# Performance work log

Measured on AMD Instinct MI355X. Metric: run time of the kernel, lower is better.

The kernel has to match this reference:

```python
import jax, jax.numpy as jnp
import numpy as np

V, E, H, O = 50000, 300, 512, 5
B, T = 256, 200
PAD = 1


def _uniform(key, shape, stdv):
    return jax.random.uniform(key, shape, jnp.float32, -stdv, stdv)


def setup_inputs() -> dict:
    key = jax.random.key(0)
    ks = jax.random.split(key, 12)
    stdv = 1.0 / np.sqrt(H)
    embed = _uniform(ks[0], (V, E), 1.0)
    embed = embed.at[PAD].set(0.0)  # padding_idx=1 row is zero
    Wi = _uniform(ks[1], (H, E + H), stdv); bi = _uniform(ks[2], (H,), stdv)
    Wf = _uniform(ks[3], (H, E + H), stdv); bf = _uniform(ks[4], (H,), stdv)
    Wg = _uniform(ks[5], (H, E + H), stdv); bg = _uniform(ks[6], (H,), stdv)
    Wo = _uniform(ks[7], (H, E + H), stdv); bo = _uniform(ks[8], (H,), stdv)
    stdv_o = 1.0 / np.sqrt(H)
    W_out = _uniform(ks[9], (O, H), stdv_o); b_out = _uniform(ks[10], (O,), stdv_o)
    x = jax.random.randint(ks[11], (B, T), 0, V, dtype=jnp.int32).astype(jnp.int64)
    return {"x": x, "embed": embed, "Wi": Wi, "bi": bi, "Wf": Wf, "bf": bf,
            "Wg": Wg, "bg": bg, "Wo": Wo, "bo": bo, "W_out": W_out, "b_out": b_out}


def _forward(x, embed, Wi, bi, Wf, bf, Wg, bg, Wo, bo, W_out, b_out):
    Bm, Tm = x.shape
    Hm = Wi.shape[0]
    emb = embed[x]  # [B, T, E]

    def step(carry, e_t):
        h, c = carry
        xs = jnp.concatenate([h, e_t], axis=1)  # [B, H+E] (prev_h first, as in torch cat)
        i = jax.nn.sigmoid(xs @ Wi.T + bi)
        f = jax.nn.sigmoid(xs @ Wf.T + bf)
        o = jax.nn.sigmoid(xs @ Wo.T + bo)
        g = jnp.tanh(xs @ Wg.T + bg)
        c = f * c + i * g
        h = jnp.tanh(c) * o
        return (h, c), h

    h0 = jnp.zeros((Bm, Hm), emb.dtype)
    c0 = jnp.zeros((Bm, Hm), emb.dtype)
    (_, _), hs = jax.lax.scan(step, (h0, c0), emb.transpose(1, 0, 2))  # hs: [T, B, H]
    outputs = hs.transpose(1, 0, 2)  # [B, T, H]
    pad = (x == PAD)[:, :, None]
    outputs = jnp.where(pad, 0.0, outputs)
    lengths = jnp.sum(x != PAD, axis=1)
    idx = lengths - 1 + jnp.arange(Bm) * Tm
    final = outputs.reshape(-1, Hm)[idx]  # [B, H]
    # Dropout(p=0.5) in eval mode -> identity
    logits = final @ W_out.T + b_out
    return logits


def reference(x, embed, Wi, bi, Wf, bf, Wg, bg, Wo, bo, W_out, b_out):
    return _forward(x, embed, Wi, bi, Wf, bf, Wg, bg, Wo, bo, W_out, b_out)
```

## Files before the change

kernel.cpp:

```cpp
#include <hip/hip_runtime.h>
#include <hip/hip_bf16.h>
#include <stdint.h>

#define E_SZ 300
#define H_SZ 512
#define O_SZ 5
#define B_SZ 256
#define T_SZ 200
#define PAD_IDX 1

#define KH 512
#define KE 320
#define KTOT 832
#define XS_W 812
#define NK 26
#define NKH 16
#define NKE 10

#define NRG 8
#define ROWS 32
#define NSPLIT 32
#define NW 16
#define WGS 256
#define THREADS 512

#define HROW_PAD 520
#define HROW_B 1040
#define HBUF_HALF (B_SZ * H_SZ)

typedef __bf16  bf16x8 __attribute__((ext_vector_type(8)));
typedef float   f32x4  __attribute__((ext_vector_type(4)));
typedef uint32_t u32x4 __attribute__((ext_vector_type(4)));

__device__ __forceinline__ float fsig(float x) { return 1.0f / (1.0f + __expf(-x)); }
__device__ __forceinline__ float ftanh_(float x) {
    float ax = fabsf(x);
    float e  = __expf(-2.0f * ax);
    float r  = (1.0f - e) / (1.0f + e);
    return x < 0.0f ? -r : r;
}


__global__ void k_pack(const float* __restrict__ Wi, const float* __restrict__ Wf,
                       const float* __restrict__ Wg, const float* __restrict__ Wo,
                       __hip_bfloat16* __restrict__ Wp) {
    int idx = blockIdx.x * blockDim.x + threadIdx.x;
    int total = 4 * H_SZ * KTOT;
    for (int i = idx; i < total; i += gridDim.x * blockDim.x) {
        int k  = i % KTOT;
        int gn = i / KTOT;
        int g = gn >> 9, n = gn & 511;
        const float* W = (g == 0) ? Wi : (g == 1) ? Wf : (g == 2) ? Wg : Wo;
        float v = 0.0f;
        if (k < KH) v = W[n * XS_W + k];
        else { int e = k - KH; if (e < E_SZ) v = W[n * XS_W + KH + e]; }
        Wp[(size_t)gn * KTOT + k] = __float2bfloat16(v);
    }
}

__global__ void k_gather(const int* __restrict__ x, const float* __restrict__ embed,
                         __hip_bfloat16* __restrict__ ebf) {
    int cid = blockIdx.x * blockDim.x + threadIdx.x;
    const int nch = T_SZ * B_SZ * (KE / 8);
    if (cid >= nch) return;
    int ch = cid % (KE / 8);
    int tb = cid / (KE / 8);
    int b = tb % B_SZ;
    int t = tb / B_SZ;
    int row = x[b * T_SZ + t];
    const float* er = embed + (size_t)row * E_SZ;
    __hip_bfloat16 v[8];
    int e0 = ch * 8;
#pragma unroll
    for (int j = 0; j < 8; ++j) {
        int e = e0 + j;
        float f = (e < E_SZ) ? er[e] : 0.0f;
        v[j] = __float2bfloat16(f);
    }
    *reinterpret_cast<ulonglong2*>(ebf + ((size_t)t * B_SZ + b) * KE + e0) =
        *reinterpret_cast<const ulonglong2*>(v);
}

__global__ void k_misc(const int* __restrict__ x, float* __restrict__ final_h,
                       int* __restrict__ tcap, int* __restrict__ flags,
                       int* __restrict__ cns) {
    int tid = blockIdx.x * blockDim.x + threadIdx.x;
    int n = gridDim.x * blockDim.x;
    for (int i = tid; i < B_SZ * H_SZ; i += n) final_h[i] = 0.0f;
    if (tid < NRG * NSPLIT) flags[tid] = 0;
    if (tid < 16) cns[tid] = 0;
    if (tid < B_SZ) {
        int len = 0;
        for (int t = 0; t < T_SZ; ++t) len += (x[tid * T_SZ + t] != PAD_IDX);
        int tf = (len > 0) ? (len - 1) : 0;
        tcap[tid] = (x[tid * T_SZ + tf] == PAD_IDX) ? -1 : tf;
    }
}

__global__ void __launch_bounds__(THREADS, 2)
k_lstm(const __hip_bfloat16* __restrict__ Wp, const __hip_bfloat16* __restrict__ ebf,
       const float* __restrict__ bi, const float* __restrict__ bfv,
       const float* __restrict__ bg, const float* __restrict__ bo,
       __hip_bfloat16* __restrict__ hbuf, float* __restrict__ final_h,
       const int* __restrict__ tcap, int* __restrict__ flags,
       int* __restrict__ cns) {
    __shared__ __align__(16) __hip_bfloat16 h_lds[ROWS * HROW_PAD];
    __shared__ float pre_lds[4][ROWS][NW + 1];
    __shared__ int s_meta[3];

    const int tid  = threadIdx.x;
    const int wave = tid >> 6;
    const int lane = tid & 63;
    const int l15  = lane & 15;
    const int l4   = lane >> 4;
    const int g    = wave & 3;
    const int rh   = wave >> 2;

    if (tid == 0) {
        uint32_t xcc;
        asm volatile("s_getreg_b32 %0, hwreg(HW_REG_XCC_ID)" : "=s"(xcc));
        xcc &= 7;
        int ticket = __hip_atomic_fetch_add(&cns[xcc], 1, __ATOMIC_RELAXED,
                                            __HIP_MEMORY_SCOPE_AGENT);
        __hip_atomic_fetch_add(&cns[8], 1, __ATOMIC_RELEASE,
                               __HIP_MEMORY_SCOPE_AGENT);
        while (__hip_atomic_load(&cns[8], __ATOMIC_RELAXED,
                                 __HIP_MEMORY_SCOPE_AGENT) < WGS)
            __builtin_amdgcn_s_sleep(8);
        (void)__hip_atomic_load(&cns[8], __ATOMIC_ACQUIRE,
                                __HIP_MEMORY_SCOPE_AGENT);
        int bal = 1;
        for (int i = 0; i < 8; ++i)
            bal &= (__hip_atomic_load(&cns[i], __ATOMIC_RELAXED,
                                      __HIP_MEMORY_SCOPE_AGENT) == NSPLIT);
        s_meta[0] = bal ? (int)xcc : (int)(blockIdx.x & 7);
        s_meta[1] = bal ? ticket : (int)(blockIdx.x >> 3);
        s_meta[2] = bal;
    }
    __syncthreads();
    const int rg   = s_meta[0];
    const int ns   = s_meta[1];
    const int fast = s_meta[2];
    const int b0   = rg * ROWS;
    const int n0   = ns * NW;

    bf16x8 wreg[NK];
    {
        const __hip_bfloat16* wB =
            Wp + ((size_t)(g * H_SZ + n0 + l15)) * KTOT + l4 * 8;
#pragma unroll
        for (int kk = 0; kk < NK; ++kk)
            wreg[kk] = *reinterpret_cast<const bf16x8*>(wB + kk * 32);
    }

    const int er  = tid >> 3;
    const int ec  = (tid & 7) * 2;
    const int enn = n0 + ec;
    const int ebb = b0 + er;
    float c0r = 0.f, c1r = 0.f;
    float bi0 = 0, bf0 = 0, bg0 = 0, bo0 = 0, bi1 = 0, bf1 = 0, bg1 = 0, bo1 = 0;
    int tc = -2;
    if (tid < 256) {
        bi0 = bi[enn];     bf0 = bfv[enn];     bg0 = bg[enn];     bo0 = bo[enn];
        bi1 = bi[enn + 1]; bf1 = bfv[enn + 1]; bg1 = bg[enn + 1]; bo1 = bo[enn + 1];
        tc = tcap[ebb];
    }

    int* const fpoll = flags + rg * NSPLIT + (lane & 31);
    int* const fmine = flags + rg * NSPLIT + ns;
    char* const lw   = (char*)(&h_lds[0]) + (wave * 4) * HROW_B;
    const char* hl_a = (const char*)(&h_lds[0]) + (rh * 16 + l15) * HROW_B + l4 * 16;

#pragma unroll 1
    for (int t = 0; t < T_SZ; ++t) {
        f32x4 acc0 = {0.f, 0.f, 0.f, 0.f};
        f32x4 acc1 = {0.f, 0.f, 0.f, 0.f};
        const __hip_bfloat16* ea =
            ebf + ((size_t)t * B_SZ + b0 + rh * 16 + l15) * KE + l4 * 8;
#pragma unroll
        for (int kk = 0; kk < NKE; ++kk) {
            bf16x8 a = *reinterpret_cast<const bf16x8*>(ea + kk * 32);
            if (kk & 1) acc1 = __builtin_amdgcn_mfma_f32_16x16x32_bf16(a, wreg[NKH + kk], acc1, 0, 0, 0);
            else        acc0 = __builtin_amdgcn_mfma_f32_16x16x32_bf16(a, wreg[NKH + kk], acc0, 0, 0, 0);
        }
        if (t > 0) {
            const uint32_t want = (uint32_t)t;
            uint32_t fv;
            if (fast) {
                for (;;) {
                    asm volatile("global_load_dword %0, %1, off sc0\n\t"
                                 "s_waitcnt vmcnt(0)"
                                 : "=&v"(fv)
                                 : "v"((uint64_t)(uintptr_t)fpoll) : "memory");
                    if (__all(fv >= want)) break;
                    __builtin_amdgcn_s_sleep(1);
                }
            } else {
                for (;;) {
                    fv = (uint32_t)__hip_atomic_load(fpoll, __ATOMIC_RELAXED,
                                                     __HIP_MEMORY_SCOPE_AGENT);
                    if (__all(fv >= want)) break;
                    __builtin_amdgcn_s_sleep(2);
                }
            }
            const char* hb = (const char*)hbuf +
                             (size_t)((t - 1) & 1) * (HBUF_HALF * 2);
            if (fast) {
                u32x4 q0, q1, q2, q3;
                const char* dp = hb + (size_t)(b0 + wave * 4) * 1024 + lane * 16;
                asm volatile(
                    "global_load_dwordx4 %0, %4, off sc0\n\t"
                    "global_load_dwordx4 %1, %4, off offset:1024 sc0\n\t"
                    "global_load_dwordx4 %2, %4, off offset:2048 sc0\n\t"
                    "global_load_dwordx4 %3, %4, off offset:3072 sc0\n\t"
                    "s_waitcnt vmcnt(0)"
                    : "=&v"(q0), "=&v"(q1), "=&v"(q2), "=&v"(q3)
                    : "v"((uint64_t)(uintptr_t)dp) : "memory");
                *reinterpret_cast<u32x4*>(lw + lane * 16)              = q0;
                *reinterpret_cast<u32x4*>(lw + HROW_B + lane * 16)     = q1;
                *reinterpret_cast<u32x4*>(lw + 2 * HROW_B + lane * 16) = q2;
                *reinterpret_cast<u32x4*>(lw + 3 * HROW_B + lane * 16) = q3;
            } else {
                uint32_t dep = fv;
                asm volatile("" : "+v"(dep));
                const uint64_t* qp =
                    (const uint64_t*)(hb + (size_t)(b0 + wave * 4) * 1024) +
                    lane + (dep >> 16);
#pragma unroll
                for (int k = 0; k < 4; ++k) {
                    uint64_t a = __hip_atomic_load(qp + k * 128, __ATOMIC_RELAXED,
                                                   __HIP_MEMORY_SCOPE_AGENT);
                    uint64_t b = __hip_atomic_load(qp + k * 128 + 64, __ATOMIC_RELAXED,
                                                   __HIP_MEMORY_SCOPE_AGENT);
                    *reinterpret_cast<uint64_t*>(lw + k * HROW_B + lane * 8)       = a;
                    *reinterpret_cast<uint64_t*>(lw + k * HROW_B + 512 + lane * 8) = b;
                }
            }
            __syncthreads();
#pragma unroll
            for (int kk = 0; kk < NKH; ++kk) {
                bf16x8 a = *reinterpret_cast<const bf16x8*>(hl_a + kk * 64);
                if (kk & 1) acc1 = __builtin_amdgcn_mfma_f32_16x16x32_bf16(a, wreg[kk], acc1, 0, 0, 0);
                else        acc0 = __builtin_amdgcn_mfma_f32_16x16x32_bf16(a, wreg[kk], acc0, 0, 0, 0);
            }
        }
        f32x4 acc = acc0 + acc1;
#pragma unroll
        for (int j = 0; j < 4; ++j)
            pre_lds[g][rh * 16 + l4 * 4 + j][l15] = acc[j];
        __syncthreads();
        if (tid < 256) {
            float pi0 = pre_lds[0][er][ec]     + bi0;
            float pf_ = pre_lds[1][er][ec]     + bf0;
            float pg0 = pre_lds[2][er][ec]     + bg0;
            float po0 = pre_lds[3][er][ec]     + bo0;
            float pi1 = pre_lds[0][er][ec + 1] + bi1;
            float pf1 = pre_lds[1][er][ec + 1] + bf1;
            float pg1 = pre_lds[2][er][ec + 1] + bg1;
            float po1 = pre_lds[3][er][ec + 1] + bo1;
            float i0 = fsig(pi0), f0 = fsig(pf_), g0v = ftanh_(pg0), o0 = fsig(po0);
            float i1 = fsig(pi1), f1 = fsig(pf1), g1v = ftanh_(pg1), o1 = fsig(po1);
            c0r = f0 * c0r + i0 * g0v;
            c1r = f1 * c1r + i1 * g1v;
            float h0 = ftanh_(c0r) * o0;
            float h1 = ftanh_(c1r) * o1;
            uint32_t pk =
                (uint32_t)__builtin_bit_cast(uint16_t, __float2bfloat16(h0)) |
                ((uint32_t)__builtin_bit_cast(uint16_t, __float2bfloat16(h1)) << 16);
            uint32_t* hw = (uint32_t*)((char*)hbuf +
                           (size_t)(t & 1) * (HBUF_HALF * 2) +
                           ((size_t)ebb * H_SZ + enn) * 2);
            if (fast)
                __hip_atomic_store(hw, pk, __ATOMIC_RELAXED,
                                   __HIP_MEMORY_SCOPE_WORKGROUP);
            else
                __hip_atomic_store(hw, pk, __ATOMIC_RELAXED,
                                   __HIP_MEMORY_SCOPE_AGENT);
            if (t == tc) {
                final_h[(size_t)ebb * H_SZ + enn]     = h0;
                final_h[(size_t)ebb * H_SZ + enn + 1] = h1;
            }
        }
        __syncthreads();
        if (tid == 0) {
            if (fast)
                __hip_atomic_store(fmine, t + 1, __ATOMIC_RELAXED,
                                   __HIP_MEMORY_SCOPE_WORKGROUP);
            else
                __hip_atomic_store(fmine, t + 1, __ATOMIC_RELAXED,
                                   __HIP_MEMORY_SCOPE_AGENT);
        }
    }
}

__global__ void k_out(const float* __restrict__ fin, const float* __restrict__ Wout,
                      const float* __restrict__ bout, float* __restrict__ out) {
    int b = blockIdx.x;
    int lane = threadIdx.x;
    float s0 = 0, s1 = 0, s2 = 0, s3 = 0, s4 = 0;
    const float* fr = fin + (size_t)b * H_SZ;
    for (int n = lane; n < H_SZ; n += 64) {
        float h = fr[n];
        s0 += h * Wout[0 * H_SZ + n];
        s1 += h * Wout[1 * H_SZ + n];
        s2 += h * Wout[2 * H_SZ + n];
        s3 += h * Wout[3 * H_SZ + n];
        s4 += h * Wout[4 * H_SZ + n];
    }
#pragma unroll
    for (int off = 32; off >= 1; off >>= 1) {
        s0 += __shfl_down(s0, off);
        s1 += __shfl_down(s1, off);
        s2 += __shfl_down(s2, off);
        s3 += __shfl_down(s3, off);
        s4 += __shfl_down(s4, off);
    }
    if (lane == 0) {
        out[b * O_SZ + 0] = s0 + bout[0];
        out[b * O_SZ + 1] = s1 + bout[1];
        out[b * O_SZ + 2] = s2 + bout[2];
        out[b * O_SZ + 3] = s3 + bout[3];
        out[b * O_SZ + 4] = s4 + bout[4];
    }
}

extern "C" void kernel_launch(void* const* d_in, const int* in_sizes, int n_in,
                              void* d_out, int out_size, void* d_ws, size_t ws_size,
                              hipStream_t stream) {
    const int*   x     = (const int*)d_in[0];
    const float* embed = (const float*)d_in[1];
    const float* Wi    = (const float*)d_in[2];
    const float* bi    = (const float*)d_in[3];
    const float* Wf    = (const float*)d_in[4];
    const float* bfv   = (const float*)d_in[5];
    const float* Wg    = (const float*)d_in[6];
    const float* bg    = (const float*)d_in[7];
    const float* Wo    = (const float*)d_in[8];
    const float* bo    = (const float*)d_in[9];
    const float* Wout  = (const float*)d_in[10];
    const float* bout  = (const float*)d_in[11];
    float* out = (float*)d_out;

    char* ws = (char*)d_ws;
    size_t off = 0;
    auto alloc = [&](size_t bytes) {
        void* p = ws + off;
        off = (off + bytes + 255) & ~(size_t)255;
        return p;
    };
    __hip_bfloat16* Wp   = (__hip_bfloat16*)alloc((size_t)4 * H_SZ * KTOT * 2);
    __hip_bfloat16* ebf  = (__hip_bfloat16*)alloc((size_t)T_SZ * B_SZ * KE * 2);
    __hip_bfloat16* hbuf = (__hip_bfloat16*)alloc((size_t)2 * HBUF_HALF * 2);
    float* finh          = (float*)alloc((size_t)B_SZ * H_SZ * 4);
    int*   tcap          = (int*)alloc((size_t)B_SZ * 4);
    int*   flags         = (int*)alloc((size_t)NRG * NSPLIT * 4);
    int*   cns           = (int*)alloc((size_t)16 * 4);
    (void)ws_size; (void)in_sizes; (void)n_in; (void)out_size;

    k_pack<<<832, 256, 0, stream>>>(Wi, Wf, Wg, Wo, Wp);
    k_gather<<<(T_SZ * B_SZ * (KE / 8) + 255) / 256, 256, 0, stream>>>(x, embed, ebf);
    k_misc<<<128, 256, 0, stream>>>(x, finh, tcap, flags, cns);

    void* args[] = { &Wp, &ebf, &bi, &bfv, &bg, &bo, &hbuf, &finh, &tcap,
                     &flags, &cns };
    hipLaunchCooperativeKernel((void*)k_lstm, dim3(WGS), dim3(THREADS), args, 0, stream);

    k_out<<<B_SZ, 64, 0, stream>>>(finh, Wout, bout, out);
}
```

Measured before the change: 877.9 us.

## Interleave gate weights per column and compute LSTM cell in-register via shuffles

Repacks the weight matrix so the four gates of each hidden column are adjacent, and switches the partition to 16 row-groups of 16 batch rows with 32 columns each. MFMA outputs are transposed across lanes with xor-shuffles so each lane holds i/f/g/o for one element, removing the pre-activation LDS staging and one barrier per step. Flag polling moves to a single wave followed by a barrier, and hidden-state stores become 16-bit volatile writes. This halves the h rows each workgroup loads per step but doubles the number of groups that must synchronise. The slow-path LDS writes include a redundant, oddly computed store.

Result: slower. 1.004 ms (+14.4%).

```diff
diff --git a/kernel.cpp b/kernel.cpp
--- a/kernel.cpp
+++ b/kernel.cpp
@@ -17,10 +17,10 @@
 #define NKH 16
 #define NKE 10
 
-#define NRG 8
-#define ROWS 32
-#define NSPLIT 32
-#define NW 16
+#define NRG 16
+#define ROWS 16
+#define NSPLIT 16
+#define NW 32
 #define WGS 256
 #define THREADS 512
 
@@ -47,14 +47,14 @@
     int idx = blockIdx.x * blockDim.x + threadIdx.x;
     int total = 4 * H_SZ * KTOT;
     for (int i = idx; i < total; i += gridDim.x * blockDim.x) {
-        int k  = i % KTOT;
-        int gn = i / KTOT;
-        int g = gn >> 9, n = gn & 511;
+        int k   = i % KTOT;
+        int gnp = i / KTOT;
+        int n = gnp >> 2, g = gnp & 3;
         const float* W = (g == 0) ? Wi : (g == 1) ? Wf : (g == 2) ? Wg : Wo;
         float v = 0.0f;
         if (k < KH) v = W[n * XS_W + k];
         else { int e = k - KH; if (e < E_SZ) v = W[n * XS_W + KH + e]; }
-        Wp[(size_t)gn * KTOT + k] = __float2bfloat16(v);
+        Wp[(size_t)gnp * KTOT + k] = __float2bfloat16(v);
     }
 }
 
@@ -105,16 +105,15 @@
        const int* __restrict__ tcap, int* __restrict__ flags,
        int* __restrict__ cns) {
     __shared__ __align__(16) __hip_bfloat16 h_lds[ROWS * HROW_PAD];
-    __shared__ float pre_lds[4][ROWS][NW + 1];
     __shared__ int s_meta[3];
 
     const int tid  = threadIdx.x;
-    const int wave = tid >> 6;
+    const int w    = tid >> 6;
     const int lane = tid & 63;
     const int l15  = lane & 15;
     const int l4   = lane >> 4;
-    const int g    = wave & 3;
-    const int rh   = wave >> 2;
+    const int cl   = l15 >> 2;
+    const int p    = l15 & 3;
 
     if (tid == 0) {
         uint32_t xcc;
@@ -132,9 +131,9 @@
         int bal = 1;
         for (int i = 0; i < 8; ++i)
             bal &= (__hip_atomic_load(&cns[i], __ATOMIC_RELAXED,
-                                      __HIP_MEMORY_SCOPE_AGENT) == NSPLIT);
-        s_meta[0] = bal ? (int)xcc : (int)(blockIdx.x & 7);
-        s_meta[1] = bal ? ticket : (int)(blockIdx.x >> 3);
+                                      __HIP_MEMORY_SCOPE_AGENT) == 32);
+        s_meta[0] = bal ? (int)(xcc * 2 + (ticket >> 4)) : (int)(blockIdx.x >> 4);
+        s_meta[1] = bal ? (ticket & 15) : (int)(blockIdx.x & 15);
         s_meta[2] = bal;
     }
     __syncthreads();
@@ -147,36 +146,31 @@
     bf16x8 wreg[NK];
     {
         const __hip_bfloat16* wB =
-            Wp + ((size_t)(g * H_SZ + n0 + l15)) * KTOT + l4 * 8;
+            Wp + ((size_t)(n0 * 4 + w * 16 + l15)) * KTOT + l4 * 8;
 #pragma unroll
         for (int kk = 0; kk < NK; ++kk)
             wreg[kk] = *reinterpret_cast<const bf16x8*>(wB + kk * 32);
     }
 
-    const int er  = tid >> 3;
-    const int ec  = (tid & 7) * 2;
-    const int enn = n0 + ec;
-    const int ebb = b0 + er;
-    float c0r = 0.f, c1r = 0.f;
-    float bi0 = 0, bf0 = 0, bg0 = 0, bo0 = 0, bi1 = 0, bf1 = 0, bg1 = 0, bo1 = 0;
-    int tc = -2;
-    if (tid < 256) {
-        bi0 = bi[enn];     bf0 = bfv[enn];     bg0 = bg[enn];     bo0 = bo[enn];
-        bi1 = bi[enn + 1]; bf1 = bfv[enn + 1]; bg1 = bg[enn + 1]; bo1 = bo[enn + 1];
-        tc = tcap[ebb];
-    }
-
-    int* const fpoll = flags + rg * NSPLIT + (lane & 31);
+    const int col   = n0 + w * 4 + cl;
+    const int row_l = l4 * 4 + p;
+    const int row   = b0 + row_l;
+    const float bib = bi[col], bfb = bfv[col], bgb = bg[col], bob = bo[col];
+    const int   tcv = tcap[row];
+    float creg = 0.0f;
+
+    int* const fpoll = flags + rg * NSPLIT + (lane & 15);
     int* const fmine = flags + rg * NSPLIT + ns;
-    char* const lw   = (char*)(&h_lds[0]) + (wave * 4) * HROW_B;
-    const char* hl_a = (const char*)(&h_lds[0]) + (rh * 16 + l15) * HROW_B + l4 * 16;
+    char* const lw   = (char*)(&h_lds[0]) + (w * 2) * HROW_B + lane * 16;
+    const char* hl_a = (const char*)(&h_lds[0]) + l15 * HROW_B + l4 * 16;
+    uint16_t* const hst0 = (uint16_t*)hbuf + (size_t)row * H_SZ + col;
 
 #pragma unroll 1
     for (int t = 0; t < T_SZ; ++t) {
         f32x4 acc0 = {0.f, 0.f, 0.f, 0.f};
         f32x4 acc1 = {0.f, 0.f, 0.f, 0.f};
         const __hip_bfloat16* ea =
-            ebf + ((size_t)t * B_SZ + b0 + rh * 16 + l15) * KE + l4 * 8;
+            ebf + ((size_t)t * B_SZ + b0 + l15) * KE + l4 * 8;
 #pragma unroll
         for (int kk = 0; kk < NKE; ++kk) {
             bf16x8 a = *reinterpret_cast<const bf16x8*>(ea + kk * 32);
@@ -184,57 +178,54 @@
             else        acc0 = __builtin_amdgcn_mfma_f32_16x16x32_bf16(a, wreg[NKH + kk], acc0, 0, 0, 0);
         }
         if (t > 0) {
-            const uint32_t want = (uint32_t)t;
-            uint32_t fv;
-            if (fast) {
-                for (;;) {
-                    asm volatile("global_load_dword %0, %1, off sc0\n\t"
-                                 "s_waitcnt vmcnt(0)"
-                                 : "=&v"(fv)
-                                 : "v"((uint64_t)(uintptr_t)fpoll) : "memory");
-                    if (__all(fv >= want)) break;
-                    __builtin_amdgcn_s_sleep(1);
-                }
-            } else {
-                for (;;) {
-                    fv = (uint32_t)__hip_atomic_load(fpoll, __ATOMIC_RELAXED,
-                                                     __HIP_MEMORY_SCOPE_AGENT);
-                    if (__all(fv >= want)) break;
-                    __builtin_amdgcn_s_sleep(2);
+            if (w == 0) {
+                const uint32_t want = (uint32_t)t;
+                uint32_t fv;
+                if (fast) {
+                    for (;;) {
+                        asm volatile("global_load_dword %0, %1, off sc0\n\t"
+                                     "s_waitcnt vmcnt(0)"
+                                     : "=&v"(fv)
+                                     : "v"((uint64_t)(uintptr_t)fpoll) : "memory");
+                        if (__all(fv >= want)) break;
+                        __builtin_amdgcn_s_sleep(1);
+                    }
+                } else {
+                    for (;;) {
+                        fv = (uint32_t)__hip_atomic_load(fpoll, __ATOMIC_ACQUIRE,
+                                                         __HIP_MEMORY_SCOPE_AGENT);
+                        if (__all(fv >= want)) break;
+                        __builtin_amdgcn_s_sleep(2);
+                    }
                 }
             }
+            __syncthreads();
             const char* hb = (const char*)hbuf +
                              (size_t)((t - 1) & 1) * (HBUF_HALF * 2);
             if (fast) {
-                u32x4 q0, q1, q2, q3;
-                const char* dp = hb + (size_t)(b0 + wave * 4) * 1024 + lane * 16;
+                u32x4 q0, q1;
+                const char* dp = hb + (size_t)(b0 + w * 2) * 1024 + lane * 16;
                 asm volatile(
-                    "global_load_dwordx4 %0, %4, off sc0\n\t"
-                    "global_load_dwordx4 %1, %4, off offset:1024 sc0\n\t"
-                    "global_load_dwordx4 %2, %4, off offset:2048 sc0\n\t"
-                    "global_load_dwordx4 %3, %4, off offset:3072 sc0\n\t"
+                    "global_load_dwordx4 %0, %2, off sc0\n\t"
+                    "global_load_dwordx4 %1, %2, off offset:1024 sc0\n\t"
                     "s_waitcnt vmcnt(0)"
-                    : "=&v"(q0), "=&v"(q1), "=&v"(q2), "=&v"(q3)
+                    : "=&v"(q0), "=&v"(q1)
                     : "v"((uint64_t)(uintptr_t)dp) : "memory");
-                *reinterpret_cast<u32x4*>(lw + lane * 16)              = q0;
-                *reinterpret_cast<u32x4*>(lw + HROW_B + lane * 16)     = q1;
-                *reinterpret_cast<u32x4*>(lw + 2 * HROW_B + lane * 16) = q2;
-                *reinterpret_cast<u32x4*>(lw + 3 * HROW_B + lane * 16) = q3;
+                *reinterpret_cast<u32x4*>(lw)          = q0;
+                *reinterpret_cast<u32x4*>(lw + HROW_B) = q1;
             } else {
-                uint32_t dep = fv;
-                asm volatile("" : "+v"(dep));
                 const uint64_t* qp =
-                    (const uint64_t*)(hb + (size_t)(b0 + wave * 4) * 1024) +
-                    lane + (dep >> 16);
-#pragma unroll
-                for (int k = 0; k < 4; ++k) {
-                    uint64_t a = __hip_atomic_load(qp + k * 128, __ATOMIC_RELAXED,
-                                                   __HIP_MEMORY_SCOPE_AGENT);
-                    uint64_t b = __hip_atomic_load(qp + k * 128 + 64, __ATOMIC_RELAXED,
-                                                   __HIP_MEMORY_SCOPE_AGENT);
-                    *reinterpret_cast<uint64_t*>(lw + k * HROW_B + lane * 8)       = a;
-                    *reinterpret_cast<uint64_t*>(lw + k * HROW_B + 512 + lane * 8) = b;
-                }
+                    (const uint64_t*)(hb + (size_t)(b0 + w * 2) * 1024) + lane;
+                uint64_t a0 = *(const volatile uint64_t*)(qp);
+                uint64_t a1 = *(const volatile uint64_t*)(qp + 64);
+                uint64_t a2 = *(const volatile uint64_t*)(qp + 128);
+                uint64_t a3 = *(const volatile uint64_t*)(qp + 192);
+                *reinterpret_cast<uint64_t*>(lw + lane * 8 - lane * 16 + lane * 8)      = a0;
+                char* lwr = (char*)(&h_lds[0]) + (w * 2) * HROW_B;
+                *reinterpret_cast<uint64_t*>(lwr + lane * 8)           = a0;
+                *reinterpret_cast<uint64_t*>(lwr + 512 + lane * 8)     = a1;
+                *reinterpret_cast<uint64_t*>(lwr + HROW_B + lane * 8)  = a2;
+                *reinterpret_cast<uint64_t*>(lwr + HROW_B + 512 + lane * 8) = a3;
             }
             __syncthreads();
 #pragma unroll
@@ -245,49 +236,29 @@
             }
         }
         f32x4 acc = acc0 + acc1;
-#pragma unroll
-        for (int j = 0; j < 4; ++j)
-            pre_lds[g][rh * 16 + l4 * 4 + j][l15] = acc[j];
-        __syncthreads();
-        if (tid < 256) {
-            float pi0 = pre_lds[0][er][ec]     + bi0;
-            float pf_ = pre_lds[1][er][ec]     + bf0;
-            float pg0 = pre_lds[2][er][ec]     + bg0;
-            float po0 = pre_lds[3][er][ec]     + bo0;
-            float pi1 = pre_lds[0][er][ec + 1] + bi1;
-            float pf1 = pre_lds[1][er][ec + 1] + bf1;
-            float pg1 = pre_lds[2][er][ec + 1] + bg1;
-            float po1 = pre_lds[3][er][ec + 1] + bo1;
-            float i0 = fsig(pi0), f0 = fsig(pf_), g0v = ftanh_(pg0), o0 = fsig(po0);
-            float i1 = fsig(pi1), f1 = fsig(pf1), g1v = ftanh_(pg1), o1 = fsig(po1);
-            c0r = f0 * c0r + i0 * g0v;
-            c1r = f1 * c1r + i1 * g1v;
-            float h0 = ftanh_(c0r) * o0;
-            float h1 = ftanh_(c1r) * o1;
-            uint32_t pk =
-                (uint32_t)__builtin_bit_cast(uint16_t, __float2bfloat16(h0)) |
-                ((uint32_t)__builtin_bit_cast(uint16_t, __float2bfloat16(h1)) << 16);
-            uint32_t* hw = (uint32_t*)((char*)hbuf +
-                           (size_t)(t & 1) * (HBUF_HALF * 2) +
-                           ((size_t)ebb * H_SZ + enn) * 2);
-            if (fast)
-                __hip_atomic_store(hw, pk, __ATOMIC_RELAXED,
-                                   __HIP_MEMORY_SCOPE_WORKGROUP);
-            else
-                __hip_atomic_store(hw, pk, __ATOMIC_RELAXED,
-                                   __HIP_MEMORY_SCOPE_AGENT);
-            if (t == tc) {
-                final_h[(size_t)ebb * H_SZ + enn]     = h0;
-                final_h[(size_t)ebb * H_SZ + enn + 1] = h1;
-            }
-        }
+        float v0 = acc[0], v1 = acc[1], v2 = acc[2], v3 = acc[3];
+        const int gb = lane & 3;
+        float t0 = __shfl_xor((gb & 1) ? v0 : v1, 1);
+        float t1 = __shfl_xor((gb & 1) ? v2 : v3, 1);
+        if (gb & 1) { v0 = t0; v2 = t1; } else { v1 = t0; v3 = t1; }
+        t0 = __shfl_xor((gb & 2) ? v0 : v2, 2);
+        t1 = __shfl_xor((gb & 2) ? v1 : v3, 2);
+        if (gb & 2) { v0 = t0; v1 = t1; } else { v2 = t0; v3 = t1; }
+        float ig = fsig(v0 + bib);
+        float fg = fsig(v1 + bfb);
+        float gg = ftanh_(v2 + bgb);
+        float og = fsig(v3 + bob);
+        creg = fg * creg + ig * gg;
+        float hv = ftanh_(creg) * og;
+        uint16_t hu = __builtin_bit_cast(uint16_t, __float2bfloat16(hv));
+        *(volatile uint16_t*)(hst0 + (size_t)(t & 1) * HBUF_HALF) = hu;
+        if (t == tcv) final_h[(size_t)row * H_SZ + col] = hv;
         __syncthreads();
         if (tid == 0) {
             if (fast)
-                __hip_atomic_store(fmine, t + 1, __ATOMIC_RELAXED,
-                                   __HIP_MEMORY_SCOPE_WORKGROUP);
+                *(volatile int*)fmine = t + 1;
             else
-                __hip_atomic_store(fmine, t + 1, __ATOMIC_RELAXED,
+                __hip_atomic_store(fmine, t + 1, __ATOMIC_RELEASE,
                                    __HIP_MEMORY_SCOPE_AGENT);
         }
     }
```
